# Optimization experiments

Hardware: AMD Instinct MI355X
Metric: run time of the kernel (lower is better)

Reference implementation:

```python
import jax, jax.numpy as jnp
import numpy as np
import math

N_HEADS = 16
D_HEAD = 64
D_MODEL = 1024
ROPE_THETA = 10000.0


def setup_inputs() -> dict:
    key = jax.random.key(0)
    k1, k2, k3 = jax.random.split(key, 3)
    B, T = 2, 2048
    x = jax.random.normal(k1, (B, T, D_MODEL), dtype=jnp.float32)
    # torch Linear(in, out) weight has shape (out, in); store transposed (in, out)
    # so forward is x @ w. Scale like default init to keep activations sane.
    w_qkv = jax.random.normal(k2, (D_MODEL, 3 * D_MODEL), dtype=jnp.float32) / math.sqrt(D_MODEL)
    w_o = jax.random.normal(k3, (D_MODEL, D_MODEL), dtype=jnp.float32) / math.sqrt(D_MODEL)
    return {"x": x, "w_qkv": w_qkv, "w_o": w_o}


def _build_rope(T, dtype):
    inv_freq = 1.0 / (ROPE_THETA ** (jnp.arange(0, D_HEAD, 2, dtype=jnp.float32) / D_HEAD))
    t = jnp.arange(T, dtype=jnp.float32)
    freqs = jnp.outer(t, inv_freq)            # [T, D_HEAD/2]
    emb = jnp.concatenate([freqs, freqs], -1)  # [T, D_HEAD]
    return jnp.cos(emb).astype(dtype), jnp.sin(emb).astype(dtype)


def _apply_rope(x, cos, sin):
    # x: [B, T, H, D_HEAD]; cos/sin broadcast as [1, T, 1, D_HEAD]
    x1, x2 = jnp.split(x, 2, axis=-1)
    rotated = jnp.concatenate([-x2, x1], axis=-1)
    return x * cos + rotated * sin


def reference(x, w_qkv, w_o):
    B, T, D = x.shape
    qkv = (x @ w_qkv).reshape(B, T, 3, N_HEADS, D_HEAD)
    q, k, v = qkv[:, :, 0], qkv[:, :, 1], qkv[:, :, 2]  # [B, T, H, Dh]
    cos, sin = _build_rope(T, x.dtype)
    cos = cos[None, :, None, :]
    sin = sin[None, :, None, :]
    q = _apply_rope(q, cos, sin)
    k = _apply_rope(k, cos, sin)
    scale = 1.0 / math.sqrt(D_HEAD)
    # full [B, H, T, T] scores (faithful to the manual matmul-softmax-matmul)
    attn = jnp.einsum("bthd,bshd->bhts", q, k) * scale
    attn = jax.nn.softmax(attn, axis=-1)
    out = jnp.einsum("bhts,bshd->bthd", attn, v).reshape(B, T, D)
    return out @ w_o
```

## Files before the change

### kernel.cpp

```cpp
#include <hip/hip_runtime.h>
#include <cstdint>

typedef unsigned short ushort_t;
typedef __attribute__((ext_vector_type(8))) short v8s;
typedef __attribute__((ext_vector_type(4))) short v4s;
typedef __attribute__((ext_vector_type(2))) unsigned v2u;
typedef __attribute__((ext_vector_type(4))) float v4f;

#define MFMA(a, b, c) __builtin_amdgcn_mfma_f32_16x16x32_bf16(a, b, c, 0, 0, 0)
#define QSCALE 0.18033688011112042f

#define GLL(gp, lp) __builtin_amdgcn_global_load_lds(                        \
    (const __attribute__((address_space(1))) void*)(gp),                     \
    (__attribute__((address_space(3))) void*)(lp), 16, 0, 0)

#define WAIT_LGKM0() __builtin_amdgcn_s_waitcnt(0xc07f)

__device__ __forceinline__ float bf2f(ushort_t u) {
    union { unsigned u; float f; } x; x.u = ((unsigned)u) << 16; return x.f;
}
__device__ __forceinline__ short f2bf(float f) {
    union { float f; unsigned u; } x; x.f = f;
    unsigned r = x.u + 0x7fffu + ((x.u >> 16) & 1u);
    return (short)(r >> 16);
}

__global__ __launch_bounds__(256) void prep(const void* __restrict__ xin,
                                            const void* __restrict__ w1,
                                            const void* __restrict__ w2,
                                            ushort_t* __restrict__ xb,
                                            ushort_t* __restrict__ out1,
                                            ushort_t* __restrict__ out2,
                                            int* __restrict__ flag,
                                            float* __restrict__ tab) {
    __shared__ ushort_t tile[64][65];
    __shared__ int cnt;
    int bid = blockIdx.x, tid = threadIdx.x;

    int isbf = 0;
    if (bid < 3072 || bid == 3328) {
        if (tid == 0) cnt = 0;
        __syncthreads();
        unsigned w = ((const unsigned*)xin)[tid];
        int e = (w >> 7) & 0xFF;
        int hit = ((e >= 96 && e <= 135) || (w & 0xFFFFu) == 0) ? 1 : 0;
        atomicAdd(&cnt, hit);
        __syncthreads();
        isbf = (cnt >= 160) ? 1 : 0;
        if (bid == 3328) {
            if (tid == 0) *flag = isbf;
            return;
        }
    }

    if (bid < 2048) {
        int i = bid * 256 + tid;
        if (isbf) {
            ((v8s*)xb)[i] = ((const v8s*)xin)[i];
        } else {
            const float* xf = (const float*)xin + (size_t)i * 8;
            v8s o;
            #pragma unroll
            for (int j = 0; j < 8; ++j) o[j] = f2bf(xf[j]);
            ((v8s*)xb)[i] = o;
        }
    } else if (bid < 3072) {
        int t = bid - 2048;
        int bxl = t & 63, by = (t >> 6) * 64;
        const void* in; ushort_t* out; int C, bx;
        if (bxl < 48) { in = w1; out = out1; C = 3072; bx = bxl * 64; }
        else          { in = w2; out = out2; C = 1024; bx = (bxl - 48) * 64; }
        const int R = 1024;
        int tx = tid & 63, ty = tid >> 6;
        for (int i = ty; i < 64; i += 4) {
            size_t idx = (size_t)(by + i) * C + bx + tx;
            tile[i][tx] = isbf ? ((const ushort_t*)in)[idx]
                               : (ushort_t)f2bf(((const float*)in)[idx]);
        }
        __syncthreads();
        for (int i = ty; i < 64; i += 4) out[(size_t)(bx + i) * R + by + tx] = tile[tx][i];
    } else {
        int idx = (bid - 3072) * 256 + tid;
        int t = idx >> 5, d = idx & 31;
        float inv_freq = __expf(-(float)d * 0.28782313662425575f);
        float ang = (float)t * inv_freq;
        float sn, cs;
        sincosf(ang, &sn, &cs);
        tab[t * 64 + d]      = bf2f((ushort_t)f2bf(cs));
        tab[t * 64 + 32 + d] = bf2f((ushort_t)f2bf(sn));
    }
}

template <int MODE, int BN>
__global__ __launch_bounds__(256) void gemm_bt(const ushort_t* __restrict__ A,
                                               const ushort_t* __restrict__ BT,
                                               void* __restrict__ C,
                                               const int* __restrict__ flagp,
                                               int M, int N, int K,
                                               ushort_t* __restrict__ Qp,
                                               ushort_t* __restrict__ Kp,
                                               ushort_t* __restrict__ Vp,
                                               const float* __restrict__ tab) {
    constexpr int NJ = BN / 32;
    __shared__ __align__(16) ushort_t As[2][128 * 32];
    __shared__ __align__(16) ushort_t Bs[2][BN * 32];
    int tid = threadIdx.x;
    int lane = tid & 63;
    int lr = lane & 15, lc = lane >> 4;
    int w = tid >> 6;
    int wr = (w >> 1) * 64, wc = (w & 1) * (BN / 2);

    int nx = gridDim.x;
    int orig = blockIdx.y * nx + blockIdx.x;
    int cpx = (nx * gridDim.y) >> 3;
    int swz = (orig & 7) * cpx + (orig >> 3);
    int m0 = (swz / nx) * 128, n0 = (swz % nx) * BN;

    int c0 = tid, c1 = tid + 256;
    int r0 = c0 >> 2, s0 = c0 & 3;
    int r1 = c1 >> 2, s1 = c1 & 3;

    const ushort_t* Ag0 = A + (size_t)(m0 + r0) * K + s0 * 8;
    const ushort_t* Ag1 = A + (size_t)(m0 + r1) * K + s1 * 8;
    const ushort_t* Bg0 = BT + (size_t)(n0 + r0) * K + s0 * 8;
    const ushort_t* Bg1 = BT + (size_t)(n0 + r1) * K + s1 * 8;
    const int aoff0 = w * 512;
    const int aoff1 = 2048 + w * 512;
    const int boff0 = w * 512;
    const int boff1 = 2048 + w * 512;

    v4f acc[4][NJ] = {};

    GLL(Ag0, &As[0][aoff0]);
    GLL(Ag1, &As[0][aoff1]);
    GLL(Bg0, &Bs[0][boff0]);
    if constexpr (BN == 128) GLL(Bg1, &Bs[0][boff1]);
    __syncthreads();

    int buf = 0;
    for (int kt = 0; kt < K; kt += 32) {
        if (kt + 32 < K) {
            int nb = buf ^ 1;
            GLL(Ag0 + kt + 32, &As[nb][aoff0]);
            GLL(Ag1 + kt + 32, &As[nb][aoff1]);
            GLL(Bg0 + kt + 32, &Bs[nb][boff0]);
            if constexpr (BN == 128) GLL(Bg1 + kt + 32, &Bs[nb][boff1]);
        }

        v8s af[4], bfr[NJ];
        #pragma unroll
        for (int i = 0; i < 4; ++i)
            af[i] = *(const v8s*)(&As[buf][0] + (wr + i * 16 + lr) * 32 + lc * 8);
        #pragma unroll
        for (int j = 0; j < NJ; ++j)
            bfr[j] = *(const v8s*)(&Bs[buf][0] + (wc + j * 16 + lr) * 32 + lc * 8);
        #pragma unroll
        for (int i = 0; i < 4; ++i)
            #pragma unroll
            for (int j = 0; j < NJ; ++j)
                acc[i][j] = MFMA(af[i], bfr[j], acc[i][j]);

        __syncthreads();
        buf ^= 1;
    }

    if (MODE == 1) {
        int store_f32 = (*flagp == 0);
        #pragma unroll
        for (int i = 0; i < 4; ++i)
            #pragma unroll
            for (int j = 0; j < NJ; ++j)
                #pragma unroll
                for (int r = 0; r < 4; ++r) {
                    int row = m0 + wr + i * 16 + lc * 4 + r;
                    int col = n0 + wc + j * 16 + lr;
                    if (store_f32)
                        ((float*)C)[(size_t)row * N + col] = acc[i][j][r];
                    else
                        ((ushort_t*)C)[(size_t)row * N + col] = (ushort_t)f2bf(acc[i][j][r]);
                }
    } else {
        int region = n0 >> 10;
        int h = ((n0 & 1023) + wc) >> 6;
        if (region < 2) {
            const float sc = (region == 0) ? QSCALE : 1.0f;
            ushort_t* dst = (region == 0) ? Qp : Kp;
            #pragma unroll
            for (int i = 0; i < 4; ++i)
                #pragma unroll
                for (int j = 0; j < 2; ++j) {
                    int d = j * 16 + lr;
                    #pragma unroll
                    for (int r = 0; r < 4; ++r) {
                        int tg = m0 + wr + i * 16 + lc * 4 + r;
                        int b = tg >> 11, tt = tg & 2047;
                        float cs = tab[tt * 64 + d], sn = tab[tt * 64 + 32 + d];
                        float x1 = acc[i][j][r], x2 = acc[i][(j + 2) % NJ][r];
                        size_t base = ((size_t)(b * 16 + h) * 2048 + tt) * 64 + d;
                        dst[base]      = (ushort_t)f2bf((x1 * cs - x2 * sn) * sc);
                        dst[base + 32] = (ushort_t)f2bf((x2 * cs + x1 * sn) * sc);
                    }
                }
        } else {
            #pragma unroll
            for (int i = 0; i < 4; ++i)
                #pragma unroll
                for (int j = 0; j < NJ; ++j) {
                    int d = j * 16 + lr;
                    int tg0 = m0 + wr + i * 16 + lc * 4;
                    int b = tg0 >> 11, tt = tg0 & 2047;
                    v4s pk;
                    #pragma unroll
                    for (int r = 0; r < 4; ++r) pk[r] = f2bf(acc[i][j][r]);
                    size_t base = (size_t)(b * 16 + h) * 131072 + (size_t)(tt >> 5) * 2048
                                + (size_t)d * 32 + (tt & 31);
                    *(v4s*)(Vp + base) = pk;
                }
        }
    }
}

__global__ __launch_bounds__(256) void attn(const ushort_t* __restrict__ Qr,
                                            const ushort_t* __restrict__ Kr,
                                            const ushort_t* __restrict__ Vt,
                                            ushort_t* __restrict__ AO) {
    __shared__ __align__(16) char lds[36864];
    int tid = threadIdx.x, lane = tid & 63, W = tid >> 6;
    int lr = lane & 15, lc = lane >> 4;
    int qsub = W & 1, sh = W >> 1;
    int L = blockIdx.x;
    int bh = (L & 7) * 4 + ((L >> 3) & 3);
    int qt = L >> 5;
    int q0 = qt * 128 + qsub * 64;
    int b = bh >> 4, h = bh & 15;
    const ushort_t* Qb = Qr + ((size_t)bh * 2048 + q0) * 64;
    const ushort_t* Kb = Kr + (size_t)bh * 131072 + (size_t)sh * 65536;
    const ushort_t* Vb = Vt + (size_t)bh * 131072 + (size_t)sh * 65536;
    ushort_t* KsG = (ushort_t*)(lds + sh * 16384);
    ushort_t* VsG = (ushort_t*)(lds + sh * 16384 + 8192);

    int gt = tid & 127;
    int c0 = gt, c1 = gt + 128;
    int kr0 = c0 >> 3, kc0 = c0 & 7, kr1 = c1 >> 3, kc1 = c1 & 7;
    const ushort_t* Kg0 = Kb + (size_t)kr0 * 64 + kc0 * 8;
    const ushort_t* Kg1 = Kb + (size_t)kr1 * 64 + kc1 * 8;
    int kl0 = kr0 * 64 + (kc0 ^ (kr0 & 7)) * 8;
    int kl1 = kr1 * 64 + (kc1 ^ (kr1 & 7)) * 8;
    const ushort_t* Vg0 = Vb + (size_t)c0 * 8;
    const ushort_t* Vg1 = Vb + (size_t)c1 * 8;
    int vl0 = c0 * 8, vl1 = c1 * 8;

    int blr = (lr >> 2) * 8 + (lr & 3);

    v8s qf[4][2];
    #pragma unroll
    for (int jq = 0; jq < 4; ++jq)
        #pragma unroll
        for (int kk = 0; kk < 2; ++kk)
            qf[jq][kk] = *(const v8s*)(Qb + (size_t)(jq * 16 + lr) * 64 + kk * 32 + lc * 8);

    v4f o[4][4] = {};
    float li[4] = {0.f, 0.f, 0.f, 0.f};

    v8s ka = *(const v8s*)(Kg0), kb2 = *(const v8s*)(Kg1);
    v8s va = *(const v8s*)(Vg0), vb2 = *(const v8s*)(Vg1);
    *(v8s*)(KsG + kl0) = ka;
    *(v8s*)(KsG + kl1) = kb2;
    *(v8s*)(VsG + vl0) = va;
    *(v8s*)(VsG + vl1) = vb2;
    ka  = *(const v8s*)(Kg0 + 2048);
    kb2 = *(const v8s*)(Kg1 + 2048);
    va  = *(const v8s*)(Vg0 + 2048);
    vb2 = *(const v8s*)(Vg1 + 2048);
    __syncthreads();

    #pragma unroll 1
    for (int t = 0; t < 32; ++t) {
        int p = t & 1;
        const ushort_t* Kl = KsG + p * 2048;
        const ushort_t* Vl = VsG + p * 2048;

        v8s kf[2][2], vf[4];
        #pragma unroll
        for (int hh = 0; hh < 2; ++hh) {
            int rn = blr + hh * 4;
            int sw = hh * 4 + (lr & 3);
            #pragma unroll
            for (int kk = 0; kk < 2; ++kk)
                kf[hh][kk] = *(const v8s*)(Kl + rn * 64 + (((kk * 4 + lc) ^ sw) * 8));
        }
        #pragma unroll
        for (int i = 0; i < 4; ++i)
            vf[i] = *(const v8s*)(Vl + (i * 16 + lr) * 32 + lc * 8);

        v4f St[2][4] = {};
        __builtin_amdgcn_s_setprio(1);
        #pragma unroll
        for (int hh = 0; hh < 2; ++hh)
            #pragma unroll
            for (int jq = 0; jq < 4; ++jq) {
                St[hh][jq] = MFMA(kf[hh][0], qf[jq][0], St[hh][jq]);
                St[hh][jq] = MFMA(kf[hh][1], qf[jq][1], St[hh][jq]);
            }
        __builtin_amdgcn_s_setprio(0);

        if (t + 1 < 32) {
            ushort_t* Kn = KsG + (p ^ 1) * 2048;
            ushort_t* Vn = VsG + (p ^ 1) * 2048;
            *(v8s*)(Kn + kl0) = ka;
            *(v8s*)(Kn + kl1) = kb2;
            *(v8s*)(Vn + vl0) = va;
            *(v8s*)(Vn + vl1) = vb2;
        }
        if (t + 2 < 32) {
            ka  = *(const v8s*)(Kg0 + (size_t)(t + 2) * 2048);
            kb2 = *(const v8s*)(Kg1 + (size_t)(t + 2) * 2048);
            va  = *(const v8s*)(Vg0 + (size_t)(t + 2) * 2048);
            vb2 = *(const v8s*)(Vg1 + (size_t)(t + 2) * 2048);
        }

        v8s pf[4];
        #pragma unroll
        for (int jq = 0; jq < 4; ++jq) {
            union { unsigned u[4]; v8s v; } P;
            #pragma unroll
            for (int hh = 0; hh < 2; ++hh) {
                #pragma unroll
                for (int r = 0; r < 4; ++r) {
                    float ev = __builtin_amdgcn_exp2f(St[hh][jq][r]);
                    St[hh][jq][r] = ev;
                    li[jq] += ev;
                }
                P.u[hh * 2 + 0] = __builtin_amdgcn_perm(__float_as_uint(St[hh][jq][1]),
                                                        __float_as_uint(St[hh][jq][0]), 0x07060302u);
                P.u[hh * 2 + 1] = __builtin_amdgcn_perm(__float_as_uint(St[hh][jq][3]),
                                                        __float_as_uint(St[hh][jq][2]), 0x07060302u);
            }
            pf[jq] = P.v;
        }
        __builtin_amdgcn_s_setprio(1);
        #pragma unroll
        for (int jq = 0; jq < 4; ++jq)
            #pragma unroll
            for (int i = 0; i < 4; ++i)
                o[i][jq] = MFMA(vf[i], pf[jq], o[i][jq]);
        __builtin_amdgcn_s_setprio(0);
        WAIT_LGKM0();
        __builtin_amdgcn_s_barrier();
    }

    #pragma unroll
    for (int jq = 0; jq < 4; ++jq) {
        li[jq] += __shfl_xor(li[jq], 16);
        li[jq] += __shfl_xor(li[jq], 32);
    }
    float* MO = (float*)(lds + qsub * 17408);
    float* Ml = (float*)(lds + 34816 + qsub * 256);
    __syncthreads();
    if (sh == 1) {
        #pragma unroll
        for (int jq = 0; jq < 4; ++jq) {
            #pragma unroll
            for (int i = 0; i < 4; ++i)
                *(v4f*)(MO + (jq * 16 + lr) * 68 + i * 16 + lc * 4) = o[i][jq];
            if (lc == 0) Ml[jq * 16 + lr] = li[jq];
        }
    }
    __syncthreads();
    if (sh == 0) {
        #pragma unroll
        for (int jq = 0; jq < 4; ++jq) {
            float inv = 1.0f / (li[jq] + Ml[jq * 16 + lr]);
            int t = q0 + jq * 16 + lr;
            #pragma unroll
            for (int i = 0; i < 4; ++i) {
                v4f m = *(const v4f*)(MO + (jq * 16 + lr) * 68 + i * 16 + lc * 4);
                v4s pk;
                #pragma unroll
                for (int r = 0; r < 4; ++r) pk[r] = f2bf((o[i][jq][r] + m[r]) * inv);
                *(v4s*)(AO + (size_t)(b * 2048 + t) * 1024 + h * 64 + i * 16 + lc * 4) = pk;
            }
        }
    }
}

extern "C" void kernel_launch(void* const* d_in, const int* in_sizes, int n_in,
                              void* d_out, int out_size, void* d_ws, size_t ws_size,
                              hipStream_t stream) {
    char* ws = (char*)d_ws;
    int*      flag  = (int*)ws;
    ushort_t* wqkvT = (ushort_t*)(ws + 256);
    ushort_t* woT   = (ushort_t*)(ws + 6291712);
    ushort_t* xb    = (ushort_t*)(ws + 8388864);
    ushort_t* Qr    = (ushort_t*)(ws + 16777472);
    ushort_t* Kr    = (ushort_t*)(ws + 25166080);
    ushort_t* Vt    = (ushort_t*)(ws + 33554688);
    ushort_t* AO    = (ushort_t*)(ws + 41943296);
    float*    tab   = (float*)(ws + 50331904);

    prep<<<3329, 256, 0, stream>>>(d_in[0], d_in[1], d_in[2], xb, wqkvT, woT, flag, tab);
    gemm_bt<2, 128><<<dim3(24, 32), 256, 0, stream>>>(xb, wqkvT, nullptr, flag, 4096, 3072, 1024,
                                                      Qr, Kr, Vt, tab);
    attn<<<512, 256, 0, stream>>>(Qr, Kr, Vt, AO);
    gemm_bt<1, 64><<<dim3(16, 32), 256, 0, stream>>>(AO, woT, d_out, flag, 4096, 1024, 1024,
                                                     nullptr, nullptr, nullptr, nullptr);
}
```

Before: 188.1 us.

## Add dedicated output-projection GEMM with K=64 tiles and transpose RoPE table

Replaces the generic gemm_bt call for the output projection with a specialized gemm_o kernel. The new kernel uses 64-wide K tiles (16 iterations instead of 32), an XOR-swizzled LDS layout, fewer barriers per unit of work, and higher MFMA priority. It also transposes the RoPE cos/sin table to a [d][t] layout, so the QKV epilogue fetches four consecutive-token values with one vector load instead of scattered scalar loads. The trade-off is doubled LDS usage per block, which may lower occupancy.

```diff
diff --git a/kernel.cpp b/kernel.cpp
--- a/kernel.cpp
+++ b/kernel.cpp
@@ -81,13 +81,13 @@
         for (int i = ty; i < 64; i += 4) out[(size_t)(bx + i) * R + by + tx] = tile[tx][i];
     } else {
         int idx = (bid - 3072) * 256 + tid;
-        int t = idx >> 5, d = idx & 31;
+        int d = idx >> 11, t = idx & 2047;
         float inv_freq = __expf(-(float)d * 0.28782313662425575f);
         float ang = (float)t * inv_freq;
         float sn, cs;
         sincosf(ang, &sn, &cs);
-        tab[t * 64 + d]      = bf2f((ushort_t)f2bf(cs));
-        tab[t * 64 + 32 + d] = bf2f((ushort_t)f2bf(sn));
+        tab[d * 2048 + t]         = bf2f((ushort_t)f2bf(cs));
+        tab[65536 + d * 2048 + t] = bf2f((ushort_t)f2bf(sn));
     }
 }
 
@@ -190,15 +190,16 @@
                 #pragma unroll
                 for (int j = 0; j < 2; ++j) {
                     int d = j * 16 + lr;
+                    int tg0 = m0 + wr + i * 16 + lc * 4;
+                    int b = tg0 >> 11, tt0 = tg0 & 2047;
+                    v4f cs4 = *(const v4f*)(tab + d * 2048 + tt0);
+                    v4f sn4 = *(const v4f*)(tab + 65536 + d * 2048 + tt0);
                     #pragma unroll
                     for (int r = 0; r < 4; ++r) {
-                        int tg = m0 + wr + i * 16 + lc * 4 + r;
-                        int b = tg >> 11, tt = tg & 2047;
-                        float cs = tab[tt * 64 + d], sn = tab[tt * 64 + 32 + d];
                         float x1 = acc[i][j][r], x2 = acc[i][(j + 2) % NJ][r];
-                        size_t base = ((size_t)(b * 16 + h) * 2048 + tt) * 64 + d;
-                        dst[base]      = (ushort_t)f2bf((x1 * cs - x2 * sn) * sc);
-                        dst[base + 32] = (ushort_t)f2bf((x2 * cs + x1 * sn) * sc);
+                        size_t base = ((size_t)(b * 16 + h) * 2048 + tt0 + r) * 64 + d;
+                        dst[base]      = (ushort_t)f2bf((x1 * cs4[r] - x2 * sn4[r]) * sc);
+                        dst[base + 32] = (ushort_t)f2bf((x2 * cs4[r] + x1 * sn4[r]) * sc);
                     }
                 }
         } else {
@@ -218,6 +219,101 @@
                 }
         }
     }
+}
+
+__global__ __launch_bounds__(256) void gemm_o(const ushort_t* __restrict__ A,
+                                              const ushort_t* __restrict__ BT,
+                                              void* __restrict__ C,
+                                              const int* __restrict__ flagp) {
+    constexpr int K = 1024, N = 1024;
+    __shared__ __align__(16) ushort_t As[2][128 * 64];
+    __shared__ __align__(16) ushort_t Bs[2][64 * 64];
+    int tid = threadIdx.x;
+    int lane = tid & 63;
+    int lr = lane & 15, lc = lane >> 4;
+    int w = tid >> 6;
+    int wr = (w >> 1) * 64, wc = (w & 1) * 32;
+
+    int nx = gridDim.x;
+    int orig = blockIdx.y * nx + blockIdx.x;
+    int cpx = (nx * gridDim.y) >> 3;
+    int swz = (orig & 7) * cpx + (orig >> 3);
+    int m0 = (swz / nx) * 128, n0 = (swz % nx) * 64;
+
+    const ushort_t* ag[4]; const ushort_t* bg[2];
+    int al[4], bl[2];
+    #pragma unroll
+    for (int q = 0; q < 4; ++q) {
+        int c = q * 256 + tid, r = c >> 3, p = c & 7;
+        ag[q] = A + (size_t)(m0 + r) * K + ((p ^ (r & 7)) * 8);
+        al[q] = (q * 256 + w * 64) * 8;
+    }
+    #pragma unroll
+    for (int q = 0; q < 2; ++q) {
+        int c = q * 256 + tid, r = c >> 3, p = c & 7;
+        bg[q] = BT + (size_t)(n0 + r) * K + ((p ^ (r & 7)) * 8);
+        bl[q] = (q * 256 + w * 64) * 8;
+    }
+
+    v4f acc[4][2] = {};
+
+    #pragma unroll
+    for (int q = 0; q < 4; ++q) GLL(ag[q], &As[0][al[q]]);
+    #pragma unroll
+    for (int q = 0; q < 2; ++q) GLL(bg[q], &Bs[0][bl[q]]);
+    __syncthreads();
+
+    int buf = 0;
+    for (int t = 0; t < 16; ++t) {
+        if (t + 1 < 16) {
+            int kg = (t + 1) * 64, nb = buf ^ 1;
+            #pragma unroll
+            for (int q = 0; q < 4; ++q) GLL(ag[q] + kg, &As[nb][al[q]]);
+            #pragma unroll
+            for (int q = 0; q < 2; ++q) GLL(bg[q] + kg, &Bs[nb][bl[q]]);
+        }
+
+        v8s af[4][2], bf[2][2];
+        #pragma unroll
+        for (int i = 0; i < 4; ++i)
+            #pragma unroll
+            for (int kk = 0; kk < 2; ++kk)
+                af[i][kk] = *(const v8s*)(&As[buf][0] + (wr + i * 16 + lr) * 64
+                                          + (((kk * 4 + lc) ^ (lr & 7)) * 8));
+        #pragma unroll
+        for (int j = 0; j < 2; ++j)
+            #pragma unroll
+            for (int kk = 0; kk < 2; ++kk)
+                bf[j][kk] = *(const v8s*)(&Bs[buf][0] + (wc + j * 16 + lr) * 64
+                                          + (((kk * 4 + lc) ^ (lr & 7)) * 8));
+        __builtin_amdgcn_s_setprio(1);
+        #pragma unroll
+        for (int i = 0; i < 4; ++i)
+            #pragma unroll
+            for (int j = 0; j < 2; ++j) {
+                acc[i][j] = MFMA(af[i][0], bf[j][0], acc[i][j]);
+                acc[i][j] = MFMA(af[i][1], bf[j][1], acc[i][j]);
+            }
+        __builtin_amdgcn_s_setprio(0);
+
+        __syncthreads();
+        buf ^= 1;
+    }
+
+    int store_f32 = (*flagp == 0);
+    #pragma unroll
+    for (int i = 0; i < 4; ++i)
+        #pragma unroll
+        for (int j = 0; j < 2; ++j)
+            #pragma unroll
+            for (int r = 0; r < 4; ++r) {
+                int row = m0 + wr + i * 16 + lc * 4 + r;
+                int col = n0 + wc + j * 16 + lr;
+                if (store_f32)
+                    ((float*)C)[(size_t)row * N + col] = acc[i][j][r];
+                else
+                    ((ushort_t*)C)[(size_t)row * N + col] = (ushort_t)f2bf(acc[i][j][r]);
+            }
 }
 
 __global__ __launch_bounds__(256) void attn(const ushort_t* __restrict__ Qr,
@@ -402,6 +498,5 @@
     gemm_bt<2, 128><<<dim3(24, 32), 256, 0, stream>>>(xb, wqkvT, nullptr, flag, 4096, 3072, 1024,
                                                       Qr, Kr, Vt, tab);
     attn<<<512, 256, 0, stream>>>(Qr, Kr, Vt, AO);
-    gemm_bt<1, 64><<<dim3(16, 32), 256, 0, stream>>>(AO, woT, d_out, flag, 4096, 1024, 1024,
-                                                     nullptr, nullptr, nullptr, nullptr);
-}
+    gemm_o<<<dim3(16, 32), 256, 0, stream>>>(AO, woT, d_out, flag);
+}
```

Measured after the change: 189.9 us. Within noise of the previous version (+1.0%).
